# Performance work log

Hardware: AMD Instinct MI355X
Metric: run time of the kernel (lower is better)

Reference implementation:

```python
import jax, jax.numpy as jnp
import numpy as np
import math

B, T, C, H = 4, 2048, 1024, 16
DH = C // H  # 64

def setup_inputs() -> dict:
    key = jax.random.key(0)
    k1, k2, k3 = jax.random.split(key, 3)
    x = jax.random.normal(k1, (B, T, C), dtype=jnp.float32)
    # standard RoPE angle table: [T, DH/2]
    inv_freq = 1.0 / (10000.0 ** (jnp.arange(0, DH, 2, dtype=jnp.float32) / DH))
    ang = jnp.arange(T, dtype=jnp.float32)[:, None] * inv_freq[None, :]
    cos = jnp.cos(ang)
    sin = jnp.sin(ang)
    Wqkv = jax.random.normal(k2, (3 * C, C), dtype=jnp.float32) * (C ** -0.5)
    Wo = jax.random.normal(k3, (C, C), dtype=jnp.float32) * (C ** -0.5)
    return {"x": x, "cos": cos, "sin": sin, "Wqkv": Wqkv, "Wo": Wo}

def apply_rotary(x, cos, sin):
    # x: [B,H,T,DH]; cos/sin: [T, DH/2] broadcast over B,H
    x1, x2 = x[..., ::2], x[..., 1::2]
    xr = jnp.stack([x1 * cos - x2 * sin, x1 * sin + x2 * cos], axis=-1)
    return xr.reshape(x.shape)

def reference(x, cos, sin, Wqkv, Wo):
    Bz, Tz, Cz = x.shape
    qkv = x @ Wqkv.T  # [B,T,3C]
    q, k, v = jnp.split(qkv, 3, axis=-1)
    def heads(t):
        return t.reshape(Bz, Tz, H, DH).transpose(0, 2, 1, 3)  # [B,H,T,DH]
    q, k, v = heads(q), heads(k), heads(v)
    q = apply_rotary(q, cos, sin)
    k = apply_rotary(k, cos, sin)
    attn = jnp.einsum('bhqd,bhkd->bhqk', q, k) / math.sqrt(DH)
    causal = jnp.tril(jnp.ones((Tz, Tz), dtype=bool))
    attn = jnp.where(causal, attn, jnp.float32(-jnp.inf))
    attn = jax.nn.softmax(attn, axis=-1)
    y = jnp.einsum('bhqk,bhkd->bhqd', attn, v)
    y = y.transpose(0, 2, 1, 3).reshape(Bz, Tz, Cz)
    return y @ Wo.T
```

## Files before the change

### kernel.cpp

```cpp
#include <hip/hip_runtime.h>
#include <math.h>

#define Bz 4
#define Tz 2048
#define Cz 1024
#define Hz 16
#define DHz 64
#define Mz (Bz*Tz)

typedef __attribute__((ext_vector_type(8))) short short8;
typedef __attribute__((ext_vector_type(4))) float f32x4;
typedef __attribute__((ext_vector_type(2))) float flt2;
typedef __attribute__((ext_vector_type(4))) float flt4;
typedef unsigned long long u64;

__device__ inline unsigned short f2bf(float f){
  union { float f; unsigned int u; } x; x.f = f;
  unsigned int r = x.u + 0x7fffu + ((x.u >> 16) & 1u);
  return (unsigned short)(r >> 16);
}
__device__ inline float bf2f(unsigned short b){
  union { unsigned int u; float f; } x; x.u = ((unsigned int)b) << 16; return x.f;
}
__device__ inline unsigned int packbf2(float lo, float hi){
  union { float f; unsigned int u; } a, b; a.f = lo; b.f = hi;
  return __builtin_amdgcn_perm(b.u, a.u, 0x07060302u);
}
__device__ inline u64 pack4bf(float a, float b, float c, float d){
  return (u64)f2bf(a) | ((u64)f2bf(b) << 16) | ((u64)f2bf(c) << 32) | ((u64)f2bf(d) << 48);
}

__device__ inline void gload_lds16(const unsigned short* g, char* l){
  __builtin_amdgcn_global_load_lds((const __attribute__((address_space(1))) unsigned int*)g,
                                   (__attribute__((address_space(3))) unsigned int*)l,
                                   16, 0, 0);
}

#define NXE 8388608
#define NW1 3145728
__global__ __launch_bounds__(256) void cvt_all(const float* __restrict__ x,
                                               const float* __restrict__ wq,
                                               const float* __restrict__ wo,
                                               unsigned short* __restrict__ xb,
                                               unsigned short* __restrict__ wqb,
                                               unsigned short* __restrict__ wob){
  int i = (blockIdx.x * 256 + threadIdx.x) * 4;
  const float* s; unsigned short* d;
  if (i < NXE){ s = x + i; d = xb + i; }
  else if (i < NXE + NW1){ s = wq + (i - NXE); d = wqb + (i - NXE); }
  else { s = wo + (i - NXE - NW1); d = wob + (i - NXE - NW1); }
  flt4 v = *(const flt4*)s;
  *(u64*)d = pack4bf(v.x, v.y, v.z, v.w);
}

template<int SWAP>
__device__ __forceinline__ void gemm_core(const unsigned short* __restrict__ As0,
                                          const unsigned short* __restrict__ Bs0,
                                          char* At, char* Bt,
                                          int tid, int wid, int l16, int lg, int wr, int wc,
                                          f32x4 acc[4][4])
{
  const int srow = tid >> 3;
  const int scol = (tid & 7) ^ (srow & 7);
  for (int kt = 0; kt < 16; ++kt){
    const unsigned short* As = As0 + kt * 64;
    const unsigned short* Bs = Bs0 + kt * 64;
    #pragma unroll
    for (int it = 0; it < 4; ++it){
      gload_lds16(As + (size_t)(it * 32 + srow) * 1024 + scol * 8, At + it * 4096 + wid * 1024);
      gload_lds16(Bs + (size_t)(it * 32 + srow) * 1024 + scol * 8, Bt + it * 4096 + wid * 1024);
    }
    __syncthreads();
    #pragma unroll
    for (int ks = 0; ks < 2; ++ks){
      short8 af[4], bf[4];
      #pragma unroll
      for (int mt = 0; mt < 4; ++mt){
        int row = wr * 64 + mt * 16 + l16;
        af[mt] = *(const short8*)(At + row * 128 + (((ks * 4 + lg) ^ (row & 7)) << 4));
      }
      #pragma unroll
      for (int nt = 0; nt < 4; ++nt){
        int row = wc * 64 + nt * 16 + l16;
        bf[nt] = *(const short8*)(Bt + row * 128 + (((ks * 4 + lg) ^ (row & 7)) << 4));
      }
      #pragma unroll
      for (int mt = 0; mt < 4; ++mt)
        #pragma unroll
        for (int nt = 0; nt < 4; ++nt)
          acc[mt][nt] = SWAP
            ? __builtin_amdgcn_mfma_f32_16x16x32_bf16(bf[nt], af[mt], acc[mt][nt], 0, 0, 0)
            : __builtin_amdgcn_mfma_f32_16x16x32_bf16(af[mt], bf[nt], acc[mt][nt], 0, 0, 0);
    }
    __syncthreads();
  }
}

__global__ __launch_bounds__(256)
void gemm_qkv(const unsigned short* __restrict__ A, const unsigned short* __restrict__ Bw,
              unsigned short* __restrict__ qd, unsigned short* __restrict__ kd,
              unsigned short* __restrict__ vd,
              const float* __restrict__ cosb, const float* __restrict__ sinb)
{
  __shared__ __align__(16) char lds[32768];
  char* At = lds; char* Bt = lds + 16384;

  const int nb = blockIdx.x, mb = blockIdx.y;
  const int m0 = mb * 128, n0 = nb * 128;

  const int tid  = threadIdx.x;
  const int lane = tid & 63, wid = tid >> 6;
  const int l16  = lane & 15, lg = lane >> 4;
  const int wr   = wid >> 1, wc = wid & 1;
  const int part = n0 >> 10;

  f32x4 acc[4][4] = {};

  if (part < 2){
    gemm_core<1>(A + (size_t)m0 * 1024, Bw + (size_t)n0 * 1024, At, Bt,
                 tid, wid, l16, lg, wr, wc, acc);
    unsigned short* dst = part ? kd : qd;
    const float qs = part ? 1.0f : 0.125f * 1.4426950408889634f;
    #pragma unroll
    for (int mt = 0; mt < 4; ++mt){
      int m = m0 + wr * 64 + mt * 16 + l16;
      int b = m >> 11, t = m & 2047;
      const float* cb = cosb + t * 32;
      const float* sb = sinb + t * 32;
      #pragma unroll
      for (int nt = 0; nt < 4; ++nt){
        int n4 = (n0 & 1023) + wc * 64 + nt * 16 + lg * 4;
        int h = n4 >> 6, d0 = n4 & 63;
        flt2 c = *(const flt2*)(cb + (d0 >> 1));
        flt2 s = *(const flt2*)(sb + (d0 >> 1));
        float x0 = acc[mt][nt][0], x1 = acc[mt][nt][1];
        float x2 = acc[mt][nt][2], x3 = acc[mt][nt][3];
        float r0 = (x0 * c.x - x1 * s.x) * qs;
        float r1 = (x0 * s.x + x1 * c.x) * qs;
        float r2 = (x2 * c.y - x3 * s.y) * qs;
        float r3 = (x2 * s.y + x3 * c.y) * qs;
        *(u64*)(dst + (((size_t)(b * Hz + h)) * Tz + t) * DHz + d0) = pack4bf(r0, r1, r2, r3);
      }
    }
  } else {
    gemm_core<0>(A + (size_t)m0 * 1024, Bw + (size_t)n0 * 1024, At, Bt,
                 tid, wid, l16, lg, wr, wc, acc);
    #pragma unroll
    for (int mt = 0; mt < 4; ++mt)
      #pragma unroll
      for (int nt = 0; nt < 4; ++nt){
        int m = m0 + wr * 64 + mt * 16 + lg * 4;
        int n = (n0 & 1023) + wc * 64 + nt * 16 + l16;
        int h = n >> 6, d = n & 63;
        int b = m >> 11, t = m & 2047;
        *(u64*)(vd + (((size_t)(b * Hz + h)) * DHz + d) * Tz + t)
          = pack4bf(acc[mt][nt][0], acc[mt][nt][1], acc[mt][nt][2], acc[mt][nt][3]);
      }
  }
}

__global__ __launch_bounds__(256)
void gemm_out(const unsigned short* __restrict__ A, const unsigned short* __restrict__ Bw,
              float* __restrict__ outf)
{
  __shared__ __align__(16) char lds[32768];
  char* At = lds; char* Bt = lds + 16384;

  const int nb = blockIdx.x, mb = blockIdx.y;
  const int m0 = mb * 128, n0 = nb * 128;

  const int tid  = threadIdx.x;
  const int lane = tid & 63, wid = tid >> 6;
  const int l16  = lane & 15, lg = lane >> 4;
  const int wr   = wid >> 1, wc = wid & 1;

  f32x4 acc[4][4] = {};
  gemm_core<1>(A + (size_t)m0 * 1024, Bw + (size_t)n0 * 1024, At, Bt,
               tid, wid, l16, lg, wr, wc, acc);

  #pragma unroll
  for (int mt = 0; mt < 4; ++mt){
    int m = m0 + wr * 64 + mt * 16 + l16;
    #pragma unroll
    for (int nt = 0; nt < 4; ++nt){
      int n = n0 + wc * 64 + nt * 16 + lg * 4;
      *(f32x4*)(outf + (size_t)m * 1024 + n) = acc[mt][nt];
    }
  }
}

__global__ __launch_bounds__(512)
void attn_fwd(const unsigned short* __restrict__ qh, const unsigned short* __restrict__ kh,
              const unsigned short* __restrict__ vt, unsigned short* __restrict__ y)
{
  __shared__ __align__(16) char lds[49152];
  const int tid  = threadIdx.x;
  const int lane = tid & 63, wid = tid >> 6;
  const int l16  = lane & 15, lg = lane >> 4;
  const int bh   = blockIdx.x;
  const int qt   = 15 - blockIdx.y;
  const int q0   = qt * 128;

  const size_t base = (size_t)bh * Tz * DHz;
  const unsigned short* qb = qh + base;
  const unsigned short* kb = kh + base;
  const unsigned short* vb = vt + base;

  const int qrow = q0 + wid * 16 + l16;
  short8 qf[2];
  qf[0] = *(const short8*)(qb + (size_t)qrow * DHz + 0  + lg * 8);
  qf[1] = *(const short8*)(qb + (size_t)qrow * DHz + 32 + lg * 8);

  const int x07 = l16 & 7;
  const int fo0 = l16 * 128 + (((0 + lg) ^ x07) << 4);
  const int fo1 = l16 * 128 + (((4 + lg) ^ x07) << 4);
  char* const Pb = (char*)lds + 32768 + wid * 2048;
  int pw[4], prd[2];
  #pragma unroll
  for (int nt = 0; nt < 4; ++nt)
    pw[nt] = l16 * 128 + ((((nt << 1) + (lg >> 1)) ^ x07) << 4) + ((lg & 1) << 3);
  prd[0] = fo0; prd[1] = fo1;

  const int srow = tid >> 3;
  const int scol = (tid & 7) ^ (srow & 7);
  const int kOff = srow * DHz + scol * 8;
  const size_t vOff = (size_t)srow * Tz + scol * 8;

  auto STAGE = [&](int kt, int c){
    gload_lds16(kb + (size_t)kt * 64 * DHz + kOff, (char*)lds + c * 8192 + tid * 16);
    gload_lds16(vb + (size_t)kt * 64 + vOff, (char*)lds + 16384 + c * 8192 + tid * 16);
  };

  short8 ones;
  #pragma unroll
  for (int j = 0; j < 8; ++j) ones[j] = (short)0x3F80;

  f32x4 o[4] = {};
  f32x4 lsum = {};
  float m_r = -INFINITY;

  auto TILE = [&](bool diag, int kt, const char* KL, const char* VL){
    f32x4 s[4] = {};
    __builtin_amdgcn_s_setprio(1);
    #pragma unroll
    for (int nt = 0; nt < 4; ++nt){
      short8 kf = *(const short8*)(KL + fo0 + nt * 2048);
      s[nt] = __builtin_amdgcn_mfma_f32_16x16x32_bf16(kf, qf[0], s[nt], 0, 0, 0);
    }
    #pragma unroll
    for (int nt = 0; nt < 4; ++nt){
      short8 kf = *(const short8*)(KL + fo1 + nt * 2048);
      s[nt] = __builtin_amdgcn_mfma_f32_16x16x32_bf16(kf, qf[1], s[nt], 0, 0, 0);
    }
    __builtin_amdgcn_s_setprio(0);

    if (diag){
      #pragma unroll
      for (int nt = 0; nt < 4; ++nt)
        #pragma unroll
        for (int r = 0; r < 4; ++r){
          int kv = kt * 64 + nt * 16 + lg * 4 + r;
          if (kv > qrow) s[nt][r] = -INFINITY;
        }
    }

    float mx = fmaxf(fmaxf(fmaxf(fmaxf(s[0][0], s[0][1]), fmaxf(s[0][2], s[0][3])),
                           fmaxf(fmaxf(s[1][0], s[1][1]), fmaxf(s[1][2], s[1][3]))),
                     fmaxf(fmaxf(fmaxf(s[2][0], s[2][1]), fmaxf(s[2][2], s[2][3])),
                           fmaxf(fmaxf(s[3][0], s[3][1]), fmaxf(s[3][2], s[3][3]))));
    mx = fmaxf(mx, __shfl_xor(mx, 16));
    mx = fmaxf(mx, __shfl_xor(mx, 32));

    if (!__all(mx - m_r <= 8.0f)){
      float mn = fmaxf(m_r, mx);
      float al = __builtin_amdgcn_exp2f(m_r - mn);
      #pragma unroll
      for (int nt = 0; nt < 4; ++nt)
        #pragma unroll
        for (int i = 0; i < 4; ++i) o[nt][i] *= al;
      #pragma unroll
      for (int i = 0; i < 4; ++i) lsum[i] *= al;
      m_r = mn;
    }

    #pragma unroll
    for (int nt = 0; nt < 4; ++nt){
      float p0 = __builtin_amdgcn_exp2f(s[nt][0] - m_r);
      float p1 = __builtin_amdgcn_exp2f(s[nt][1] - m_r);
      float p2 = __builtin_amdgcn_exp2f(s[nt][2] - m_r);
      float p3 = __builtin_amdgcn_exp2f(s[nt][3] - m_r);
      *(u64*)(Pb + pw[nt]) = (u64)packbf2(p0, p1) | ((u64)packbf2(p2, p3) << 32);
    }

    __builtin_amdgcn_s_setprio(1);
    #pragma unroll
    for (int ks = 0; ks < 2; ++ks){
      short8 pa = *(const short8*)(Pb + prd[ks]);
      lsum = __builtin_amdgcn_mfma_f32_16x16x32_bf16(ones, pa, lsum, 0, 0, 0);
      const int fo = ks ? fo1 : fo0;
      #pragma unroll
      for (int nt = 0; nt < 4; ++nt){
        short8 vf = *(const short8*)(VL + fo + nt * 2048);
        o[nt] = __builtin_amdgcn_mfma_f32_16x16x32_bf16(vf, pa, o[nt], 0, 0, 0);
      }
    }
    __builtin_amdgcn_s_setprio(0);
  };

  int cur = 0;
  STAGE(0, 0);
  __syncthreads();

  const int last = 2 * qt + 1;
  for (int kt = 0; kt < last; ++kt){
    STAGE(kt + 1, cur ^ 1);
    TILE(kt >= 2 * qt, kt, (const char*)lds + cur * 8192,
         (const char*)lds + 16384 + cur * 8192);
    __syncthreads();
    cur ^= 1;
  }
  TILE(true, last, (const char*)lds + cur * 8192,
       (const char*)lds + 16384 + cur * 8192);

  const int b = bh >> 4, h = bh & 15;
  unsigned short* yb = y + ((size_t)b * Tz + qrow) * Cz + h * 64 + lg * 4;
  float inv = 1.f / lsum[0];
  #pragma unroll
  for (int nt = 0; nt < 4; ++nt)
    *(u64*)(yb + nt * 16) = pack4bf(o[nt][0] * inv, o[nt][1] * inv,
                                    o[nt][2] * inv, o[nt][3] * inv);
}

extern "C" void kernel_launch(void* const* d_in, const int* in_sizes, int n_in,
                              void* d_out, int out_size, void* d_ws, size_t ws_size,
                              hipStream_t stream)
{
  const float* x    = (const float*)d_in[0];
  const float* cosb = (const float*)d_in[1];
  const float* sinb = (const float*)d_in[2];
  const float* Wqkv = (const float*)d_in[3];
  const float* Wo   = (const float*)d_in[4];
  float* out = (float*)d_out;

  char* ws = (char*)d_ws;
  unsigned short* xb    = (unsigned short*)(ws);
  unsigned short* ybuf  = xb;
  unsigned short* wqkvb = (unsigned short*)(ws + 16777216);
  unsigned short* wob   = (unsigned short*)(ws + 23068672);
  unsigned short* qhb   = (unsigned short*)(ws + 25165824);
  unsigned short* khb   = (unsigned short*)(ws + 41943040);
  unsigned short* vtb   = (unsigned short*)(ws + 58720256);

  cvt_all<<<12288, 256, 0, stream>>>(x, Wqkv, Wo, xb, wqkvb, wob);

  gemm_qkv<<<dim3(24, 64), 256, 0, stream>>>(xb, wqkvb, qhb, khb, vtb, cosb, sinb);

  attn_fwd<<<dim3(64, 16), 512, 0, stream>>>(qhb, khb, vtb, ybuf);

  gemm_out<<<dim3(8, 64), 256, 0, stream>>>(ybuf, wob, out);
}
```

Measured before the change: 262.2 us.

## Switch attention to 32x32x16 MFMA with 4 waves of 32 query rows

```diff
diff --git a/kernel.cpp b/kernel.cpp
--- a/kernel.cpp
+++ b/kernel.cpp
@@ -10,6 +10,7 @@
 
 typedef __attribute__((ext_vector_type(8))) short short8;
 typedef __attribute__((ext_vector_type(4))) float f32x4;
+typedef __attribute__((ext_vector_type(16))) float f32x16;
 typedef __attribute__((ext_vector_type(2))) float flt2;
 typedef __attribute__((ext_vector_type(4))) float flt4;
 typedef unsigned long long u64;
@@ -189,37 +190,37 @@
   }
 }
 
-__global__ __launch_bounds__(512)
+__global__ __launch_bounds__(256)
 void attn_fwd(const unsigned short* __restrict__ qh, const unsigned short* __restrict__ kh,
               const unsigned short* __restrict__ vt, unsigned short* __restrict__ y)
 {
-  __shared__ __align__(16) char lds[49152];
+  __shared__ __align__(16) char lds[50176];
   const int tid  = threadIdx.x;
   const int lane = tid & 63, wid = tid >> 6;
-  const int l16  = lane & 15, lg = lane >> 4;
+  const int l31  = lane & 31, hi = lane >> 5;
   const int bh   = blockIdx.x;
   const int qt   = 15 - blockIdx.y;
-  const int q0   = qt * 128;
+  const int q0w  = qt * 128 + wid * 32;
+  const int qg   = q0w + l31;
 
   const size_t base = (size_t)bh * Tz * DHz;
   const unsigned short* qb = qh + base;
   const unsigned short* kb = kh + base;
   const unsigned short* vb = vt + base;
 
-  const int qrow = q0 + wid * 16 + l16;
-  short8 qf[2];
-  qf[0] = *(const short8*)(qb + (size_t)qrow * DHz + 0  + lg * 8);
-  qf[1] = *(const short8*)(qb + (size_t)qrow * DHz + 32 + lg * 8);
-
-  const int x07 = l16 & 7;
-  const int fo0 = l16 * 128 + (((0 + lg) ^ x07) << 4);
-  const int fo1 = l16 * 128 + (((4 + lg) ^ x07) << 4);
-  char* const Pb = (char*)lds + 32768 + wid * 2048;
-  int pw[4], prd[2];
-  #pragma unroll
-  for (int nt = 0; nt < 4; ++nt)
-    pw[nt] = l16 * 128 + ((((nt << 1) + (lg >> 1)) ^ x07) << 4) + ((lg & 1) << 3);
-  prd[0] = fo0; prd[1] = fo1;
+  short8 qf[4];
+  #pragma unroll
+  for (int ks = 0; ks < 4; ++ks)
+    qf[ks] = *(const short8*)(qb + (size_t)qg * DHz + ks * 16 + hi * 8);
+
+  int foK[4];
+  #pragma unroll
+  for (int ks = 0; ks < 4; ++ks)
+    foK[ks] = l31 * 128 + ((((ks << 1) + hi) ^ (l31 & 7)) << 4);
+
+  char* const Pt = (char*)lds + 32768 + wid * 4352;
+  const int pwb = l31 * 136 + hi * 8;
+  const int prb = l31 * 136 + hi * 16;
 
   const int srow = tid >> 3;
   const int scol = (tid & 7) ^ (srow & 7);
@@ -227,108 +228,142 @@
   const size_t vOff = (size_t)srow * Tz + scol * 8;
 
   auto STAGE = [&](int kt, int c){
-    gload_lds16(kb + (size_t)kt * 64 * DHz + kOff, (char*)lds + c * 8192 + tid * 16);
-    gload_lds16(vb + (size_t)kt * 64 + vOff, (char*)lds + 16384 + c * 8192 + tid * 16);
+    const unsigned short* Ks = kb + (size_t)kt * 64 * DHz;
+    const unsigned short* Vs = vb + kt * 64;
+    #pragma unroll
+    for (int it = 0; it < 2; ++it){
+      gload_lds16(Ks + kOff + it * 32 * DHz,
+                  (char*)lds + c * 8192 + it * 4096 + wid * 1024);
+      gload_lds16(Vs + vOff + (size_t)it * 32 * Tz,
+                  (char*)lds + 16384 + c * 8192 + it * 4096 + wid * 1024);
+    }
   };
 
   short8 ones;
   #pragma unroll
   for (int j = 0; j < 8; ++j) ones[j] = (short)0x3F80;
 
-  f32x4 o[4] = {};
-  f32x4 lsum = {};
+  f32x16 o0 = {}, o1 = {}, ls = {};
   float m_r = -INFINITY;
-
-  auto TILE = [&](bool diag, int kt, const char* KL, const char* VL){
-    f32x4 s[4] = {};
-    __builtin_amdgcn_s_setprio(1);
-    #pragma unroll
-    for (int nt = 0; nt < 4; ++nt){
-      short8 kf = *(const short8*)(KL + fo0 + nt * 2048);
-      s[nt] = __builtin_amdgcn_mfma_f32_16x16x32_bf16(kf, qf[0], s[nt], 0, 0, 0);
-    }
-    #pragma unroll
-    for (int nt = 0; nt < 4; ++nt){
-      short8 kf = *(const short8*)(KL + fo1 + nt * 2048);
-      s[nt] = __builtin_amdgcn_mfma_f32_16x16x32_bf16(kf, qf[1], s[nt], 0, 0, 0);
-    }
-    __builtin_amdgcn_s_setprio(0);
-
-    if (diag){
-      #pragma unroll
-      for (int nt = 0; nt < 4; ++nt)
-        #pragma unroll
-        for (int r = 0; r < 4; ++r){
-          int kv = kt * 64 + nt * 16 + lg * 4 + r;
-          if (kv > qrow) s[nt][r] = -INFINITY;
-        }
-    }
-
-    float mx = fmaxf(fmaxf(fmaxf(fmaxf(s[0][0], s[0][1]), fmaxf(s[0][2], s[0][3])),
-                           fmaxf(fmaxf(s[1][0], s[1][1]), fmaxf(s[1][2], s[1][3]))),
-                     fmaxf(fmaxf(fmaxf(s[2][0], s[2][1]), fmaxf(s[2][2], s[2][3])),
-                           fmaxf(fmaxf(s[3][0], s[3][1]), fmaxf(s[3][2], s[3][3]))));
-    mx = fmaxf(mx, __shfl_xor(mx, 16));
-    mx = fmaxf(mx, __shfl_xor(mx, 32));
-
-    if (!__all(mx - m_r <= 8.0f)){
-      float mn = fmaxf(m_r, mx);
-      float al = __builtin_amdgcn_exp2f(m_r - mn);
-      #pragma unroll
-      for (int nt = 0; nt < 4; ++nt)
-        #pragma unroll
-        for (int i = 0; i < 4; ++i) o[nt][i] *= al;
-      #pragma unroll
-      for (int i = 0; i < 4; ++i) lsum[i] *= al;
-      m_r = mn;
-    }
-
-    #pragma unroll
-    for (int nt = 0; nt < 4; ++nt){
-      float p0 = __builtin_amdgcn_exp2f(s[nt][0] - m_r);
-      float p1 = __builtin_amdgcn_exp2f(s[nt][1] - m_r);
-      float p2 = __builtin_amdgcn_exp2f(s[nt][2] - m_r);
-      float p3 = __builtin_amdgcn_exp2f(s[nt][3] - m_r);
-      *(u64*)(Pb + pw[nt]) = (u64)packbf2(p0, p1) | ((u64)packbf2(p2, p3) << 32);
-    }
-
-    __builtin_amdgcn_s_setprio(1);
-    #pragma unroll
-    for (int ks = 0; ks < 2; ++ks){
-      short8 pa = *(const short8*)(Pb + prd[ks]);
-      lsum = __builtin_amdgcn_mfma_f32_16x16x32_bf16(ones, pa, lsum, 0, 0, 0);
-      const int fo = ks ? fo1 : fo0;
-      #pragma unroll
-      for (int nt = 0; nt < 4; ++nt){
-        short8 vf = *(const short8*)(VL + fo + nt * 2048);
-        o[nt] = __builtin_amdgcn_mfma_f32_16x16x32_bf16(vf, pa, o[nt], 0, 0, 0);
-      }
-    }
-    __builtin_amdgcn_s_setprio(0);
-  };
 
   int cur = 0;
   STAGE(0, 0);
   __syncthreads();
 
   const int last = 2 * qt + 1;
-  for (int kt = 0; kt < last; ++kt){
-    STAGE(kt + 1, cur ^ 1);
-    TILE(kt >= 2 * qt, kt, (const char*)lds + cur * 8192,
-         (const char*)lds + 16384 + cur * 8192);
-    __syncthreads();
-    cur ^= 1;
-  }
-  TILE(true, last, (const char*)lds + cur * 8192,
-       (const char*)lds + 16384 + cur * 8192);
+  for (int kt = 0; kt <= last; ++kt){
+    if (kt < last) STAGE(kt + 1, cur ^ 1);
+
+    const int act = q0w + 31 - 64 * kt;
+    const int nkb = act < 0 ? 0 : (act >= 32 ? 2 : 1);
+    if (nkb){
+      const char* KL = (const char*)lds + cur * 8192;
+      const char* VL = (const char*)lds + 16384 + cur * 8192;
+
+      f32x16 s0 = {}, s1 = {};
+      __builtin_amdgcn_s_setprio(1);
+      #pragma unroll
+      for (int ks = 0; ks < 4; ++ks){
+        short8 kf = *(const short8*)(KL + foK[ks]);
+        s0 = __builtin_amdgcn_mfma_f32_32x32x16_bf16(kf, qf[ks], s0, 0, 0, 0);
+      }
+      if (nkb > 1){
+        #pragma unroll
+        for (int ks = 0; ks < 4; ++ks){
+          short8 kf = *(const short8*)(KL + 4096 + foK[ks]);
+          s1 = __builtin_amdgcn_mfma_f32_32x32x16_bf16(kf, qf[ks], s1, 0, 0, 0);
+        }
+      }
+      __builtin_amdgcn_s_setprio(0);
+
+      if (64 * kt + 31 > q0w){
+        #pragma unroll
+        for (int r = 0; r < 16; ++r){
+          int kv = 64 * kt + (r & 3) + 8 * (r >> 2) + 4 * hi;
+          if (kv > qg) s0[r] = -INFINITY;
+        }
+      }
+      if (nkb > 1 && 64 * kt + 63 > q0w){
+        #pragma unroll
+        for (int r = 0; r < 16; ++r){
+          int kv = 64 * kt + 32 + (r & 3) + 8 * (r >> 2) + 4 * hi;
+          if (kv > qg) s1[r] = -INFINITY;
+        }
+      }
+
+      float a0 = fmaxf(fmaxf(s0[0], s0[1]),  fmaxf(s0[2], s0[3]));
+      float a1 = fmaxf(fmaxf(s0[4], s0[5]),  fmaxf(s0[6], s0[7]));
+      float a2 = fmaxf(fmaxf(s0[8], s0[9]),  fmaxf(s0[10], s0[11]));
+      float a3 = fmaxf(fmaxf(s0[12], s0[13]), fmaxf(s0[14], s0[15]));
+      float mx = fmaxf(fmaxf(a0, a1), fmaxf(a2, a3));
+      if (nkb > 1){
+        float b0 = fmaxf(fmaxf(s1[0], s1[1]),  fmaxf(s1[2], s1[3]));
+        float b1 = fmaxf(fmaxf(s1[4], s1[5]),  fmaxf(s1[6], s1[7]));
+        float b2 = fmaxf(fmaxf(s1[8], s1[9]),  fmaxf(s1[10], s1[11]));
+        float b3 = fmaxf(fmaxf(s1[12], s1[13]), fmaxf(s1[14], s1[15]));
+        mx = fmaxf(mx, fmaxf(fmaxf(b0, b1), fmaxf(b2, b3)));
+      }
+      mx = fmaxf(mx, __shfl_xor(mx, 32));
+
+      if (!__all(mx - m_r <= 8.0f)){
+        float mn = fmaxf(m_r, mx);
+        float al = __builtin_amdgcn_exp2f(m_r - mn);
+        #pragma unroll
+        for (int j = 0; j < 16; ++j){ o0[j] *= al; o1[j] *= al; ls[j] *= al; }
+        m_r = mn;
+      }
+
+      #pragma unroll
+      for (int k = 0; k < 4; ++k){
+        float p0 = __builtin_amdgcn_exp2f(s0[4*k+0] - m_r);
+        float p1 = __builtin_amdgcn_exp2f(s0[4*k+1] - m_r);
+        float p2 = __builtin_amdgcn_exp2f(s0[4*k+2] - m_r);
+        float p3 = __builtin_amdgcn_exp2f(s0[4*k+3] - m_r);
+        *(u64*)(Pt + pwb + k * 16) = (u64)packbf2(p0, p1) | ((u64)packbf2(p2, p3) << 32);
+      }
+      if (nkb > 1){
+        #pragma unroll
+        for (int k = 0; k < 4; ++k){
+          float p0 = __builtin_amdgcn_exp2f(s1[4*k+0] - m_r);
+          float p1 = __builtin_amdgcn_exp2f(s1[4*k+1] - m_r);
+          float p2 = __builtin_amdgcn_exp2f(s1[4*k+2] - m_r);
+          float p3 = __builtin_amdgcn_exp2f(s1[4*k+3] - m_r);
+          *(u64*)(Pt + pwb + 64 + k * 16) = (u64)packbf2(p0, p1) | ((u64)packbf2(p2, p3) << 32);
+        }
+      }
+
+      __builtin_amdgcn_s_setprio(1);
+      #pragma unroll
+      for (int ks = 0; ks < 4; ++ks){
+        if (ks < 2 * nkb){
+          const u64* pr = (const u64*)(Pt + prb + ks * 32);
+          union { u64 q[2]; short8 v; } pu;
+          pu.q[0] = pr[0]; pu.q[1] = pr[1];
+          short8 pf = pu.v;
+          ls = __builtin_amdgcn_mfma_f32_32x32x16_bf16(ones, pf, ls, 0, 0, 0);
+          short8 v0 = *(const short8*)(VL + foK[ks]);
+          o0 = __builtin_amdgcn_mfma_f32_32x32x16_bf16(v0, pf, o0, 0, 0, 0);
+          short8 v1 = *(const short8*)(VL + 4096 + foK[ks]);
+          o1 = __builtin_amdgcn_mfma_f32_32x32x16_bf16(v1, pf, o1, 0, 0, 0);
+        }
+      }
+      __builtin_amdgcn_s_setprio(0);
+    }
+
+    if (kt < last){ __syncthreads(); cur ^= 1; }
+  }
 
   const int b = bh >> 4, h = bh & 15;
-  unsigned short* yb = y + ((size_t)b * Tz + qrow) * Cz + h * 64 + lg * 4;
-  float inv = 1.f / lsum[0];
-  #pragma unroll
-  for (int nt = 0; nt < 4; ++nt)
-    *(u64*)(yb + nt * 16) = pack4bf(o[nt][0] * inv, o[nt][1] * inv,
-                                    o[nt][2] * inv, o[nt][3] * inv);
+  unsigned short* yb = y + ((size_t)b * Tz + qg) * Cz + h * 64;
+  float inv = 1.f / ls[0];
+  #pragma unroll
+  for (int k = 0; k < 4; ++k){
+    int d0 = 8 * k + 4 * hi;
+    *(u64*)(yb + d0)      = pack4bf(o0[4*k+0] * inv, o0[4*k+1] * inv,
+                                    o0[4*k+2] * inv, o0[4*k+3] * inv);
+    *(u64*)(yb + 32 + d0) = pack4bf(o1[4*k+0] * inv, o1[4*k+1] * inv,
+                                    o1[4*k+2] * inv, o1[4*k+3] * inv);
+  }
 }
 
 extern "C" void kernel_launch(void* const* d_in, const int* in_sizes, int n_in,
@@ -355,7 +390,7 @@
 
   gemm_qkv<<<dim3(24, 64), 256, 0, stream>>>(xb, wqkvb, qhb, khb, vtb, cosb, sinb);
 
-  attn_fwd<<<dim3(64, 16), 512, 0, stream>>>(qhb, khb, vtb, ybuf);
+  attn_fwd<<<dim3(64, 16), 256, 0, stream>>>(qhb, khb, vtb, ybuf);
 
   gemm_out<<<dim3(8, 64), 256, 0, stream>>>(ybuf, wob, out);
 }
```

After: 269.9 us. +2.9%, slower.
